# Performance work log

Hardware: AMD Instinct MI355X
Metric: run time of the kernel (lower is better)

Reference implementation:

```python
import jax, jax.numpy as jnp
import numpy as np

S, HID, H, KH, D = 2048, 3584, 28, 4, 128
G = H // KH  # GQA group size = 7
EPS = 1e-6
THETA = 1000000.0


def _rmsnorm(x, w, eps=EPS):
    v = jnp.mean(x.astype(jnp.float32) ** 2, axis=-1, keepdims=True)
    return (x * jax.lax.rsqrt(v + eps)).astype(x.dtype) * w


def setup_inputs() -> dict:
    key = jax.random.key(0)
    k1, k2, k3, k4 = jax.random.split(key, 4)
    return {
        "positions": jnp.arange(S, dtype=jnp.int32),
        "hidden_states": jax.random.normal(k1, (S, HID), dtype=jnp.float32),
        "qkv_w": jax.random.normal(k2, ((H + 2 * KH) * D, HID), dtype=jnp.float32) * (1.0 / np.sqrt(HID)),
        "qkv_b": jax.random.normal(k3, ((H + 2 * KH) * D,), dtype=jnp.float32) * 0.02,
        "q_norm_w": jnp.ones((H * D,), dtype=jnp.float32),
        "k_norm_w": jnp.ones((KH * D,), dtype=jnp.float32),
        "o_w": jax.random.normal(k4, (HID, H * D), dtype=jnp.float32) * (1.0 / np.sqrt(H * D)),
    }


def reference(positions, hidden_states, qkv_w, qkv_b, q_norm_w, k_norm_w, o_w):
    # QKV projection (fused linear, bias=True)
    qkv = hidden_states @ qkv_w.T + qkv_b  # [S, (H+2*KH)*D]
    q, k, v = jnp.split(qkv, [H * D, H * D + KH * D], axis=-1)

    # olmo-style QK RMSNorm over the full (all-heads-concatenated) q/k vectors
    q = _rmsnorm(q, q_norm_w)
    k = _rmsnorm(k, k_norm_w)

    # NeoX-style RoPE (vLLM default): rotate halves
    half = D // 2
    inv_freq = 1.0 / (THETA ** (jnp.arange(0, D, 2, dtype=jnp.float32) / D))  # [D/2]
    freqs = positions[:, None].astype(jnp.float32) * inv_freq  # [S, D/2]
    cos = jnp.cos(freqs)[:, None, :]  # [S, 1, D/2]
    sin = jnp.sin(freqs)[:, None, :]

    def rope(x, nh):
        x = x.reshape(S, nh, D)
        x1, x2 = x[..., :half], x[..., half:]
        return jnp.concatenate([x1 * cos - x2 * sin, x2 * cos + x1 * sin], axis=-1)

    q = rope(q, H)            # [S, H, D]
    k = rope(k, KH)           # [S, KH, D]
    v = v.reshape(S, KH, D)   # [S, KH, D]

    # Grouped-query causal attention
    qg = q.reshape(S, KH, G, D)
    scores = jnp.einsum('skgd,tkd->kgst', qg, k) * (D ** -0.5)  # [KH, G, S, S]
    causal = positions[:, None] >= positions[None, :]  # [S, S]
    scores = jnp.where(causal[None, None], scores, jnp.finfo(scores.dtype).min)
    probs = jax.nn.softmax(scores, axis=-1)
    attn = jnp.einsum('kgst,tkd->skgd', probs, v).reshape(S, H * D)

    # Output projection (bias=False)
    return attn @ o_w.T  # [S, HID]
```

## Files before the change

kernel.cpp:

```cpp
#include <hip/hip_runtime.h>
#include <hip/hip_bf16.h>
#include <stdint.h>

#define S_LEN 2048
#define HIDDEN 3584
#define NH 28
#define NKH 4
#define DH 128
#define NG 7
#define NQKV 4608
#define QD 3584
#define KD 512

using bf16x8 = __attribute__((ext_vector_type(8))) __bf16;
using f32x4  = __attribute__((ext_vector_type(4))) float;
using f32x16 = __attribute__((ext_vector_type(16))) float;

#define AS3(p) ((__attribute__((address_space(3))) void*)(p))
#define AS1(p) ((const __attribute__((address_space(1))) void*)(p))

__device__ __forceinline__ unsigned short f2bf(float f) {
    unsigned u = __float_as_uint(f);
    u += 0x7FFFu + ((u >> 16) & 1u);
    return (unsigned short)(u >> 16);
}
__device__ __forceinline__ unsigned cvtpk(float a, float b) {
    unsigned r;
    asm("v_cvt_pk_bf16_f32 %0, %1, %2" : "=v"(r) : "v"(a), "v"(b));
    return r;
}

__global__ void cvt2_f32_bf16(const float* __restrict__ a, unsigned short* __restrict__ oa, int na4,
                              const float* __restrict__ b, unsigned short* __restrict__ ob, int nb4) {
    int i = blockIdx.x * blockDim.x + threadIdx.x;
    const float* src;
    unsigned short* dst;
    int n;
    if (i < na4)            { src = a; dst = oa; n = i; }
    else if (i < na4 + nb4) { src = b; dst = ob; n = i - na4; }
    else return;
    float4 v = ((const float4*)src)[n];
    ushort4 o;
    o.x = f2bf(v.x); o.y = f2bf(v.y); o.z = f2bf(v.z); o.w = f2bf(v.w);
    ((ushort4*)dst)[n] = o;
}

__global__ void cvt_f32_bf16(const float* __restrict__ in,
                             unsigned short* __restrict__ out, int n4) {
    int i = blockIdx.x * blockDim.x + threadIdx.x;
    if (i >= n4) return;
    float4 v = ((const float4*)in)[i];
    ushort4 o;
    o.x = f2bf(v.x); o.y = f2bf(v.y); o.z = f2bf(v.z); o.w = f2bf(v.w);
    ((ushort4*)out)[i] = o;
}

__global__ __launch_bounds__(256) void gemm_bf16(
    const unsigned short* __restrict__ A,
    const unsigned short* __restrict__ B,
    float* __restrict__ C,
    const float* __restrict__ bias,
    int M, int N, int K)
{
    __shared__ __align__(16) unsigned char smem[2][32768];

    const int tid  = threadIdx.x;
    const int lane = tid & 63;
    const int w    = tid >> 6;
    const int lr   = lane & 15;
    const int lg   = lane >> 4;
    const int m0   = blockIdx.y * 128;
    const int n0   = blockIdx.x * 128;
    const int wm   = (w >> 1) * 64;
    const int wn   = (w & 1) * 64;

    f32x4 acc[4][4] = {};

    const int srow  = lane >> 3;
    const int scolb = 16 * ((lane & 7) ^ srow);
    const unsigned char* Ab = (const unsigned char*)A;
    const unsigned char* Bb = (const unsigned char*)B;

    auto stage = [&](int kt, int b) {
        const long kbyte = (long)kt * 128;
        #pragma unroll
        for (int i = 0; i < 4; ++i) {
            const int c   = w * 4 + i;
            const int row = c * 8 + srow;
            __builtin_amdgcn_global_load_lds(
                AS1(Ab + (long)(m0 + row) * (K * 2) + kbyte + scolb),
                AS3(&smem[b][0] + c * 1024), 16, 0, 0);
            __builtin_amdgcn_global_load_lds(
                AS1(Bb + (long)(n0 + row) * (K * 2) + kbyte + scolb),
                AS3(&smem[b][16384] + c * 1024), 16, 0, 0);
        }
    };

    stage(0, 0);
    asm volatile("s_waitcnt vmcnt(0)" ::: "memory");
    __builtin_amdgcn_s_barrier();

    const int nk = K >> 6;
    for (int kt = 0; kt < nk; ++kt) {
        const int cur = kt & 1;
        if (kt + 1 < nk) stage(kt + 1, cur ^ 1);

        const unsigned char* As = &smem[cur][0];
        const unsigned char* Bs = &smem[cur][16384];
        #pragma unroll
        for (int kk = 0; kk < 2; ++kk) {
            bf16x8 af[4], bfr[4];
            #pragma unroll
            for (int mi = 0; mi < 4; ++mi) {
                const int row  = wm + mi * 16 + lr;
                const int colb = kk * 64 + lg * 16;
                af[mi] = *(const bf16x8*)(As + row * 128 + (colb ^ ((row & 7) << 4)));
            }
            #pragma unroll
            for (int ni = 0; ni < 4; ++ni) {
                const int row  = wn + ni * 16 + lr;
                const int colb = kk * 64 + lg * 16;
                bfr[ni] = *(const bf16x8*)(Bs + row * 128 + (colb ^ ((row & 7) << 4)));
            }
            #pragma unroll
            for (int mi = 0; mi < 4; ++mi)
                #pragma unroll
                for (int ni = 0; ni < 4; ++ni)
                    acc[mi][ni] = __builtin_amdgcn_mfma_f32_16x16x32_bf16(
                        af[mi], bfr[ni], acc[mi][ni], 0, 0, 0);
        }

        asm volatile("s_waitcnt vmcnt(0)" ::: "memory");
        __builtin_amdgcn_s_barrier();
    }

    #pragma unroll
    for (int mi = 0; mi < 4; ++mi) {
        #pragma unroll
        for (int ni = 0; ni < 4; ++ni) {
            const int col = n0 + wn + ni * 16 + lr;
            const float bv = bias ? bias[col] : 0.0f;
            #pragma unroll
            for (int j = 0; j < 4; ++j) {
                const int rowg = m0 + wm + mi * 16 + lg * 4 + j;
                C[(long)rowg * N + col] = acc[mi][ni][j] + bv;
            }
        }
    }
}

__global__ __launch_bounds__(256) void qkv_post(
    const float* __restrict__ qkv,
    const int* __restrict__ positions,
    const float* __restrict__ qnw,
    const float* __restrict__ knw,
    unsigned short* __restrict__ qb,
    unsigned short* __restrict__ kb,
    unsigned short* __restrict__ vt2)
{
    const int s   = blockIdx.x;
    const int tid = threadIdx.x;
    const float* rowp = qkv + (long)s * NQKV;
    __shared__ float red[256];
    __shared__ float s_rq, s_rk;

    float aq = 0.f;
    for (int i = tid; i < QD; i += 256) { float v = rowp[i]; aq += v * v; }
    red[tid] = aq; __syncthreads();
    for (int off = 128; off > 0; off >>= 1) {
        if (tid < off) red[tid] += red[tid + off];
        __syncthreads();
    }
    if (tid == 0) s_rq = rsqrtf(red[0] / (float)QD + 1e-6f);
    __syncthreads();

    float ak = 0.f;
    for (int i = tid; i < KD; i += 256) { float v = rowp[QD + i]; ak += v * v; }
    red[tid] = ak; __syncthreads();
    for (int off = 128; off > 0; off >>= 1) {
        if (tid < off) red[tid] += red[tid + off];
        __syncthreads();
    }
    if (tid == 0) s_rk = rsqrtf(red[0] / (float)KD + 1e-6f);
    __syncthreads();

    const float rq  = s_rq, rk = s_rk * 0.08838834764831845f;
    const float pos = (float)positions[s];
    const float c_lnf = 0.21586735253866598f;

    for (int u = tid; u < NH * 64; u += 256) {
        const int h = u >> 6, j = u & 63;
        const float inv = expf(-(float)j * c_lnf);
        float sn, cs;
        sincosf(pos * inv, &sn, &cs);
        const float x1 = rowp[h * DH + j]      * rq * qnw[h * DH + j];
        const float x2 = rowp[h * DH + 64 + j] * rq * qnw[h * DH + 64 + j];
        qb[((long)h * S_LEN + s) * DH + j]      = f2bf(x1 * cs - x2 * sn);
        qb[((long)h * S_LEN + s) * DH + 64 + j] = f2bf(x2 * cs + x1 * sn);
    }
    for (int u = tid; u < NKH * 64; u += 256) {
        const int h = u >> 6, j = u & 63;
        const float inv = expf(-(float)j * c_lnf);
        float sn, cs;
        sincosf(pos * inv, &sn, &cs);
        const float x1 = rowp[QD + h * DH + j]      * rk * knw[h * DH + j];
        const float x2 = rowp[QD + h * DH + 64 + j] * rk * knw[h * DH + 64 + j];
        kb[((long)h * S_LEN + s) * DH + j]      = f2bf(x1 * cs - x2 * sn);
        kb[((long)h * S_LEN + s) * DH + 64 + j] = f2bf(x2 * cs + x1 * sn);
    }
    for (int u = tid; u < KD; u += 256) {
        const int hh = u >> 7, d = u & 127;
        vt2[(((long)hh * (S_LEN / 32) + (s >> 5)) * DH + d) * 32 + (s & 31)] =
            f2bf(rowp[QD + KD + u]);
    }
}

__global__ __launch_bounds__(512) void attn_fwd(
    const unsigned short* __restrict__ qb,
    const unsigned short* __restrict__ kb,
    const unsigned short* __restrict__ vt2,
    unsigned short* __restrict__ attnb)
{
    __shared__ __align__(16) unsigned char sK[2][8192];
    __shared__ __align__(16) unsigned char sV[2][8192];

    const int qt   = 63 - blockIdx.x;
    const int kh   = blockIdx.y;
    const int tid  = threadIdx.x;
    const int w    = tid >> 6;
    const int lane = tid & 63;
    const int lq   = lane & 31;
    const int hi   = lane >> 5;
    const int hi8  = hi * 8;
    const int hi4  = hi * 4;
    const int q0   = qt * 32;
    const int NT   = qt + 1;

    const unsigned char* kgb = (const unsigned char*)(kb + (long)kh * S_LEN * DH);
    const unsigned char* vgb = (const unsigned char*)vt2 + (long)kh * (S_LEN / 32) * 8192;

    const int ksrc_off = (((tid & 15) ^ (tid >> 4)) & 15) << 4;
    const int u        = tid & 255;
    const int vsrc_off = ((u & 3) ^ ((u >> 3) & 3)) << 4;

    const float RTHR = 8.0f;

    bf16x8 qf[8];
    if (w < 7) {
        const int h = kh * NG + w;
        const unsigned short* qrow = qb + ((long)h * S_LEN + q0 + lq) * DH;
        #pragma unroll
        for (int c = 0; c < 8; ++c)
            qf[c] = *(const bf16x8*)(qrow + c * 16 + hi8);
    }

    f32x16 o[4] = {};
    float m = -3e38f;
    float l = 0.f;

    if (tid < 256) {
        #pragma unroll
        for (int j = 0; j < 2; ++j)
            __builtin_amdgcn_global_load_lds(AS1(kgb + ((tid >> 4) + 16 * j) * 256 + ksrc_off),
                                             AS3(&sK[0][0] + w * 1024 + j * 4096), 16, 0, 0);
    } else {
        #pragma unroll
        for (int j = 0; j < 2; ++j)
            __builtin_amdgcn_global_load_lds(AS1(vgb + ((u >> 2) + 64 * j) * 64 + vsrc_off),
                                             AS3(&sV[0][0] + (w - 4) * 1024 + j * 4096), 16, 0, 0);
    }

    for (int t = 0; t < NT; ++t) {
        __syncthreads();

        if (t + 1 < NT) {
            const int b = (t + 1) & 1;
            if (tid < 256) {
                const unsigned char* ks = kgb + (long)(t + 1) * 8192;
                #pragma unroll
                for (int j = 0; j < 2; ++j)
                    __builtin_amdgcn_global_load_lds(AS1(ks + ((tid >> 4) + 16 * j) * 256 + ksrc_off),
                                                     AS3(&sK[b][0] + w * 1024 + j * 4096), 16, 0, 0);
            } else {
                const unsigned char* vs = vgb + (long)(t + 1) * 8192;
                #pragma unroll
                for (int j = 0; j < 2; ++j)
                    __builtin_amdgcn_global_load_lds(AS1(vs + ((u >> 2) + 64 * j) * 64 + vsrc_off),
                                                     AS3(&sV[b][0] + (w - 4) * 1024 + j * 4096), 16, 0, 0);
            }
        }

        if (w < 7) {
            const unsigned char* sKb = sK[t & 1];
            const unsigned char* sVb = sV[t & 1];

            bf16x8 kf[8];
            #pragma unroll
            for (int c = 0; c < 8; ++c)
                kf[c] = *(const bf16x8*)(sKb + lq * 256 + (((2 * c + hi) ^ (lq & 15)) << 4));
            f32x16 sc = {};
            #pragma unroll
            for (int c = 0; c < 8; ++c)
                sc = __builtin_amdgcn_mfma_f32_32x32x16_bf16(kf[c], qf[c], sc, 0, 0, 0);

            float s[16];
            if (t == NT - 1) {
                #pragma unroll
                for (int r = 0; r < 16; ++r) {
                    const int kr = (r & 3) + 8 * (r >> 2) + hi4;
                    s[r] = (kr > lq) ? -3e38f : sc[r];
                }
            } else {
                #pragma unroll
                for (int r = 0; r < 16; ++r) s[r] = sc[r];
            }

            float mx = s[0];
            #pragma unroll
            for (int r = 1; r < 16; ++r) mx = fmaxf(mx, s[r]);
            mx = fmaxf(mx, __shfl_xor(mx, 32));

            if (!__all(mx <= m + RTHR)) {
                const float nm  = fmaxf(m, mx);
                const float fac = __expf(m - nm);
                l *= fac;
                #pragma unroll
                for (int d0 = 0; d0 < 4; ++d0)
                    #pragma unroll
                    for (int r = 0; r < 16; ++r) o[d0][r] *= fac;
                m = nm;
            }

            float p[16];
            float ps = 0.f;
            #pragma unroll
            for (int r = 0; r < 16; ++r) {
                p[r] = __expf(s[r] - m);
                ps += p[r];
            }
            ps += __shfl_xor(ps, 32);
            l += ps;

            unsigned pa01 = cvtpk(p[0],  p[1]),  pa23 = cvtpk(p[2],  p[3]);
            unsigned pb01 = cvtpk(p[4],  p[5]),  pb23 = cvtpk(p[6],  p[7]);
            unsigned pc01 = cvtpk(p[8],  p[9]),  pc23 = cvtpk(p[10], p[11]);
            unsigned pd01 = cvtpk(p[12], p[13]), pd23 = cvtpk(p[14], p[15]);
            unsigned xa01 = __shfl_xor((int)pa01, 32), xa23 = __shfl_xor((int)pa23, 32);
            unsigned xb01 = __shfl_xor((int)pb01, 32), xb23 = __shfl_xor((int)pb23, 32);
            unsigned xc01 = __shfl_xor((int)pc01, 32), xc23 = __shfl_xor((int)pc23, 32);
            unsigned xd01 = __shfl_xor((int)pd01, 32), xd23 = __shfl_xor((int)pd23, 32);

            union { unsigned uu[4]; bf16x8 v; } pf0, pf1;
            pf0.uu[0] = hi ? xb01 : pa01;
            pf0.uu[1] = hi ? xb23 : pa23;
            pf0.uu[2] = hi ? pb01 : xa01;
            pf0.uu[3] = hi ? pb23 : xa23;
            pf1.uu[0] = hi ? xd01 : pc01;
            pf1.uu[1] = hi ? xd23 : pc23;
            pf1.uu[2] = hi ? pd01 : xc01;
            pf1.uu[3] = hi ? pd23 : xc23;

            #pragma unroll
            for (int d0 = 0; d0 < 4; ++d0) {
                const int row = d0 * 32 + lq;
                const int sw  = (lq >> 1) & 3;
                bf16x8 vf0 = *(const bf16x8*)(sVb + row * 64 + ((hi ^ sw) << 4));
                bf16x8 vf1 = *(const bf16x8*)(sVb + row * 64 + (((2 + hi) ^ sw) << 4));
                o[d0] = __builtin_amdgcn_mfma_f32_32x32x16_bf16(vf0, pf0.v, o[d0], 0, 0, 0);
                o[d0] = __builtin_amdgcn_mfma_f32_32x32x16_bf16(vf1, pf1.v, o[d0], 0, 0, 0);
            }
        }
    }

    if (w == 7) return;

    const float rl = 1.0f / l;
    unsigned short* orow = attnb + (long)(q0 + lq) * QD + (kh * NG + w) * DH;
    #pragma unroll
    for (int d0 = 0; d0 < 4; ++d0) {
        #pragma unroll
        for (int g = 0; g < 4; ++g) {
            ushort4 s4;
            s4.x = f2bf(o[d0][4 * g + 0] * rl);
            s4.y = f2bf(o[d0][4 * g + 1] * rl);
            s4.z = f2bf(o[d0][4 * g + 2] * rl);
            s4.w = f2bf(o[d0][4 * g + 3] * rl);
            *(ushort4*)(orow + d0 * 32 + 8 * g + hi4) = s4;
        }
    }
}

extern "C" void kernel_launch(void* const* d_in, const int* in_sizes, int n_in,
                              void* d_out, int out_size, void* d_ws, size_t ws_size,
                              hipStream_t stream) {
    const int*   positions = (const int*)d_in[0];
    const float* hidden    = (const float*)d_in[1];
    const float* qkv_w     = (const float*)d_in[2];
    const float* qkv_b     = (const float*)d_in[3];
    const float* qnw       = (const float*)d_in[4];
    const float* knw       = (const float*)d_in[5];
    const float* o_w       = (const float*)d_in[6];
    float* out = (float*)d_out;

    unsigned char* ws = (unsigned char*)d_ws;
    unsigned short* hb    = (unsigned short*)(ws);
    unsigned short* w1    = (unsigned short*)(ws + 14680064);
    float*          qkvf  = (float*)(ws + 47710208);
    unsigned short* qbuf  = (unsigned short*)(ws + 85458944);
    unsigned short* kbuf  = (unsigned short*)(ws + 100139008);
    unsigned short* vtb   = (unsigned short*)(ws + 102236160);
    unsigned short* attnb = (unsigned short*)(ws);
    unsigned short* w2    = (unsigned short*)(ws + 14680064);

    const int na4 = S_LEN * HIDDEN / 4;
    const int nb4 = NQKV * HIDDEN / 4;
    cvt2_f32_bf16<<<(na4 + nb4 + 255) / 256, 256, 0, stream>>>(hidden, hb, na4, qkv_w, w1, nb4);
    gemm_bf16<<<dim3(NQKV / 128, S_LEN / 128), 256, 0, stream>>>(hb, w1, qkvf, qkv_b, S_LEN, NQKV, HIDDEN);
    qkv_post<<<S_LEN, 256, 0, stream>>>(qkvf, positions, qnw, knw, qbuf, kbuf, vtb);
    attn_fwd<<<dim3(S_LEN / 32, NKH), 512, 0, stream>>>(qbuf, kbuf, vtb, attnb);
    cvt_f32_bf16<<<(HIDDEN * QD / 4 + 255) / 256, 256, 0, stream>>>(o_w, w2, HIDDEN * QD / 4);
    gemm_bf16<<<dim3(HIDDEN / 128, S_LEN / 128), 256, 0, stream>>>(attnb, w2, out, nullptr, S_LEN, HIDDEN, QD);
}
```

Before: 291.9 us.

## Replace 128x128 GEMM with larger-tile 512-thread kernel using triple-stage prefetch

Replaces the 128x128 bf16 MFMA GEMM with a templated kernel that uses 256-row tiles, 8 waves and a per-call-site N tile (192 for QKV, 128 for the output projection). This raises operand reuse per byte loaded from global memory. The prefetch now runs two tiles ahead with partial vmcnt waits. The MFMA work is split into two halves around the barrier so the next stage's loads overlap with compute, and s_setprio is raised during the MFMA blocks. In exchange it uses more LDS and registers per block and launches fewer blocks, which could hurt occupancy or tail balance.

```diff
diff --git a/kernel.cpp b/kernel.cpp
--- a/kernel.cpp
+++ b/kernel.cpp
@@ -55,95 +55,129 @@
     ((ushort4*)out)[i] = o;
 }
 
-__global__ __launch_bounds__(256) void gemm_bf16(
+template<int BN>
+__global__ __launch_bounds__(512, 2) void gemm_big(
     const unsigned short* __restrict__ A,
     const unsigned short* __restrict__ B,
     float* __restrict__ C,
     const float* __restrict__ bias,
     int M, int N, int K)
 {
-    __shared__ __align__(16) unsigned char smem[2][32768];
+    constexpr int NF    = BN / 64;
+    constexpr int WN    = BN / 4;
+    constexpr int BBLK  = BN / 8;
+    constexpr int SBLK  = 32 + BBLK;
+    constexpr int SPW   = SBLK / 8;
+    constexpr int TILEB = SBLK * 1024;
+
+    __shared__ __align__(16) unsigned char dsmem[2 * TILEB];
 
     const int tid  = threadIdx.x;
+    const int w    = tid >> 6;
     const int lane = tid & 63;
-    const int w    = tid >> 6;
     const int lr   = lane & 15;
     const int lg   = lane >> 4;
-    const int m0   = blockIdx.y * 128;
-    const int n0   = blockIdx.x * 128;
-    const int wm   = (w >> 1) * 64;
-    const int wn   = (w & 1) * 64;
-
-    f32x4 acc[4][4] = {};
-
-    const int srow  = lane >> 3;
-    const int scolb = 16 * ((lane & 7) ^ srow);
+    const int wr   = w >> 2;
+    const int wc   = w & 3;
+    const int m0   = blockIdx.y * 256;
+    const int n0   = blockIdx.x * BN;
+    const long K2  = (long)K * 2;
+
+    const int srow = lane >> 3;
+    const int scw  = 16 * ((lane & 7) ^ srow);
     const unsigned char* Ab = (const unsigned char*)A;
     const unsigned char* Bb = (const unsigned char*)B;
 
-    auto stage = [&](int kt, int b) {
-        const long kbyte = (long)kt * 128;
-        #pragma unroll
-        for (int i = 0; i < 4; ++i) {
-            const int c   = w * 4 + i;
-            const int row = c * 8 + srow;
-            __builtin_amdgcn_global_load_lds(
-                AS1(Ab + (long)(m0 + row) * (K * 2) + kbyte + scolb),
-                AS3(&smem[b][0] + c * 1024), 16, 0, 0);
-            __builtin_amdgcn_global_load_lds(
-                AS1(Bb + (long)(n0 + row) * (K * 2) + kbyte + scolb),
-                AS3(&smem[b][16384] + c * 1024), 16, 0, 0);
+    auto stage = [&](int kt, unsigned char* buf) {
+        const long kb = (long)kt * 128;
+        #pragma unroll
+        for (int j = 0; j < SPW; ++j) {
+            const int blk = w * SPW + j;
+            const unsigned char* src = (blk < 32)
+                ? Ab + (long)(m0 + blk * 8 + srow) * K2 + kb + scw
+                : Bb + (long)(n0 + (blk - 32) * 8 + srow) * K2 + kb + scw;
+            __builtin_amdgcn_global_load_lds(AS1(src), AS3(buf + blk * 1024), 16, 0, 0);
         }
     };
 
-    stage(0, 0);
-    asm volatile("s_waitcnt vmcnt(0)" ::: "memory");
+    f32x4 acc[8][NF] = {};
+
+    stage(0, dsmem);
+    stage(1, dsmem + TILEB);
+    if constexpr (SPW == 7) asm volatile("s_waitcnt vmcnt(7)" ::: "memory");
+    else                    asm volatile("s_waitcnt vmcnt(6)" ::: "memory");
     __builtin_amdgcn_s_barrier();
 
     const int nk = K >> 6;
     for (int kt = 0; kt < nk; ++kt) {
-        const int cur = kt & 1;
-        if (kt + 1 < nk) stage(kt + 1, cur ^ 1);
-
-        const unsigned char* As = &smem[cur][0];
-        const unsigned char* Bs = &smem[cur][16384];
-        #pragma unroll
-        for (int kk = 0; kk < 2; ++kk) {
-            bf16x8 af[4], bfr[4];
-            #pragma unroll
-            for (int mi = 0; mi < 4; ++mi) {
-                const int row  = wm + mi * 16 + lr;
-                const int colb = kk * 64 + lg * 16;
-                af[mi] = *(const bf16x8*)(As + row * 128 + (colb ^ ((row & 7) << 4)));
-            }
-            #pragma unroll
-            for (int ni = 0; ni < 4; ++ni) {
-                const int row  = wn + ni * 16 + lr;
-                const int colb = kk * 64 + lg * 16;
-                bfr[ni] = *(const bf16x8*)(Bs + row * 128 + (colb ^ ((row & 7) << 4)));
-            }
-            #pragma unroll
-            for (int mi = 0; mi < 4; ++mi)
-                #pragma unroll
-                for (int ni = 0; ni < 4; ++ni)
+        unsigned char* buf = dsmem + (kt & 1) * TILEB;
+        const unsigned char* As = buf;
+        const unsigned char* Bs = buf + 32768;
+
+        bf16x8 a[8][2], bfr[NF][2];
+        #pragma unroll
+        for (int mi = 0; mi < 8; ++mi) {
+            const int row = wr * 128 + mi * 16 + lr;
+            #pragma unroll
+            for (int kk = 0; kk < 2; ++kk)
+                a[mi][kk] = *(const bf16x8*)(As + row * 128 +
+                                             ((kk * 64 + lg * 16) ^ ((lr & 7) << 4)));
+        }
+        #pragma unroll
+        for (int ni = 0; ni < NF; ++ni) {
+            const int row = wc * WN + ni * 16 + lr;
+            #pragma unroll
+            for (int kk = 0; kk < 2; ++kk)
+                bfr[ni][kk] = *(const bf16x8*)(Bs + row * 128 +
+                                               ((kk * 64 + lg * 16) ^ ((lr & 7) << 4)));
+        }
+
+        __builtin_amdgcn_s_setprio(1);
+        #pragma unroll
+        for (int mi = 0; mi < 4; ++mi)
+            #pragma unroll
+            for (int ni = 0; ni < NF; ++ni)
+                #pragma unroll
+                for (int kk = 0; kk < 2; ++kk)
                     acc[mi][ni] = __builtin_amdgcn_mfma_f32_16x16x32_bf16(
-                        af[mi], bfr[ni], acc[mi][ni], 0, 0, 0);
-        }
-
-        asm volatile("s_waitcnt vmcnt(0)" ::: "memory");
+                        a[mi][kk], bfr[ni][kk], acc[mi][ni], 0, 0, 0);
+        __builtin_amdgcn_s_setprio(0);
+
+        asm volatile("s_waitcnt lgkmcnt(0)" ::: "memory");
         __builtin_amdgcn_s_barrier();
+
+        if (kt + 2 < nk) stage(kt + 2, buf);
+
+        __builtin_amdgcn_s_setprio(1);
+        #pragma unroll
+        for (int mi = 4; mi < 8; ++mi)
+            #pragma unroll
+            for (int ni = 0; ni < NF; ++ni)
+                #pragma unroll
+                for (int kk = 0; kk < 2; ++kk)
+                    acc[mi][ni] = __builtin_amdgcn_mfma_f32_16x16x32_bf16(
+                        a[mi][kk], bfr[ni][kk], acc[mi][ni], 0, 0, 0);
+        __builtin_amdgcn_s_setprio(0);
+
+        if (kt + 2 < nk) {
+            if constexpr (SPW == 7) asm volatile("s_waitcnt vmcnt(7)" ::: "memory");
+            else                    asm volatile("s_waitcnt vmcnt(6)" ::: "memory");
+        } else {
+            asm volatile("s_waitcnt vmcnt(0)" ::: "memory");
+        }
+        __builtin_amdgcn_s_barrier();
     }
 
     #pragma unroll
-    for (int mi = 0; mi < 4; ++mi) {
-        #pragma unroll
-        for (int ni = 0; ni < 4; ++ni) {
-            const int col = n0 + wn + ni * 16 + lr;
+    for (int mi = 0; mi < 8; ++mi) {
+        #pragma unroll
+        for (int ni = 0; ni < NF; ++ni) {
+            const int col = n0 + wc * WN + ni * 16 + lr;
             const float bv = bias ? bias[col] : 0.0f;
             #pragma unroll
             for (int j = 0; j < 4; ++j) {
-                const int rowg = m0 + wm + mi * 16 + lg * 4 + j;
-                C[(long)rowg * N + col] = acc[mi][ni][j] + bv;
+                const int row = m0 + wr * 128 + mi * 16 + lg * 4 + j;
+                C[(long)row * N + col] = acc[mi][ni][j] + bv;
             }
         }
     }
@@ -415,9 +449,11 @@
     const int na4 = S_LEN * HIDDEN / 4;
     const int nb4 = NQKV * HIDDEN / 4;
     cvt2_f32_bf16<<<(na4 + nb4 + 255) / 256, 256, 0, stream>>>(hidden, hb, na4, qkv_w, w1, nb4);
-    gemm_bf16<<<dim3(NQKV / 128, S_LEN / 128), 256, 0, stream>>>(hb, w1, qkvf, qkv_b, S_LEN, NQKV, HIDDEN);
+    gemm_big<192><<<dim3(NQKV / 192, S_LEN / 256), 512, 0, stream>>>(
+        hb, w1, qkvf, qkv_b, S_LEN, NQKV, HIDDEN);
     qkv_post<<<S_LEN, 256, 0, stream>>>(qkvf, positions, qnw, knw, qbuf, kbuf, vtb);
     attn_fwd<<<dim3(S_LEN / 32, NKH), 512, 0, stream>>>(qbuf, kbuf, vtb, attnb);
     cvt_f32_bf16<<<(HIDDEN * QD / 4 + 255) / 256, 256, 0, stream>>>(o_w, w2, HIDDEN * QD / 4);
-    gemm_bf16<<<dim3(HIDDEN / 128, S_LEN / 128), 256, 0, stream>>>(attnb, w2, out, nullptr, S_LEN, HIDDEN, QD);
-}
+    gemm_big<128><<<dim3(HIDDEN / 128, S_LEN / 256), 512, 0, stream>>>(
+        attnb, w2, out, nullptr, S_LEN, HIDDEN, QD);
+}
```

New measurement: 281.7 us. -3.5%, faster.
